# Kernel tuning notes

Hardware: AMD Instinct MI355X
Metric: run time of the kernel (lower is better)

The kernel has to match this reference:

```python
import jax, jax.numpy as jnp
import numpy as np

N = 8192
IN_CH = 256
HID = 256
NEG_INF = -1000000000.0


def setup_inputs() -> dict:
    key = jax.random.key(0)
    ks = jax.random.split(key, 7)
    inlayer = jax.random.normal(ks[0], (N, IN_CH), dtype=jnp.float32)
    adj_mat = jax.random.randint(ks[1], (N, N), 0, 2, dtype=jnp.int32)
    # Xavier-uniform style scales
    s0 = (6.0 / (IN_CH + HID)) ** 0.5
    s1 = (6.0 / (HID + 1)) ** 0.5
    W = jax.random.uniform(ks[2], (HID, IN_CH), jnp.float32, -s0, s0)   # conv1d.weight[:, :, 0]
    w1 = jax.random.uniform(ks[3], (1, HID), jnp.float32, -s1, s1)      # conv1d1.weight[:, :, 0]
    b1 = jax.random.uniform(ks[4], (1,), jnp.float32, -s1, s1)          # conv1d1.bias
    w2 = jax.random.uniform(ks[5], (1, HID), jnp.float32, -s1, s1)      # conv1d2.weight[:, :, 0]
    b2 = jax.random.uniform(ks[6], (1,), jnp.float32, -s1, s1)          # conv1d2.bias
    return {"inlayer": inlayer, "adj_mat": adj_mat, "W": W,
            "w1": w1, "b1": b1, "w2": w2, "b2": b2}


def reference(inlayer, adj_mat, W, w1, b1, w2, b2):
    # 1x1 conv == linear projection: in_fts [HID, N]
    in_fts = W @ inlayer.T
    f1 = (w1 @ in_fts).T + b1          # [N, 1]
    f2 = (w2 @ in_fts).T + b2          # [N, 1]
    logits = f1 + f2.T                 # [N, N] broadcast add
    bias_mat = jnp.where(adj_mat > 0, 0.0, NEG_INF).astype(logits.dtype)
    coefs = jax.nn.softmax(jax.nn.leaky_relu(logits) + bias_mat, axis=-1)
    vals = coefs @ inlayer             # [N, IN_CH]
    return vals
```

## Files before the change

### kernel.cpp

```cpp
#include <hip/hip_runtime.h>
#include <hip/hip_bf16.h>

typedef float f32x4 __attribute__((ext_vector_type(4)));
typedef __bf16 bf16x8 __attribute__((ext_vector_type(8)));

#define N 8192
#define CH 256
#define NJC 4
#define JCW (N / NJC)
#define JT 128
#define NT (JCW / JT)
#define BM 64

static constexpr size_t OFF_P1 = 0;
static constexpr size_t OFF_P2 = 32768;
static constexpr size_t OFF_T1 = 65536;
static constexpr size_t OFF_T2 = 66560;
static constexpr size_t OFF_F1 = 67584;
static constexpr size_t OFF_F2 = OFF_F1 + (size_t)N * 4;
static constexpr size_t OFF_XT = 262144;
static constexpr size_t OFF_SP = OFF_XT + (size_t)CH * N * 2;
static constexpr size_t OFF_PV = OFF_SP + (size_t)NJC * N * 4;

__global__ __launch_bounds__(256) void k1a(
    const float* __restrict__ W, const float* __restrict__ w1,
    const float* __restrict__ w2, float* __restrict__ p1, float* __restrict__ p2)
{
    int b = blockIdx.x, c = threadIdx.x;
    float a1 = 0.f, a2 = 0.f;
#pragma unroll
    for (int hh = 0; hh < 8; ++hh) {
        int h = b * 8 + hh;
        float wv = W[h * CH + c];
        a1 = __builtin_fmaf(w1[h], wv, a1);
        a2 = __builtin_fmaf(w2[h], wv, a2);
    }
    p1[b * CH + c] = a1;
    p2[b * CH + c] = a2;
}

__global__ __launch_bounds__(256) void k1b(
    const float* __restrict__ p1, const float* __restrict__ p2,
    float* __restrict__ t1, float* __restrict__ t2)
{
    int c = threadIdx.x;
    float a1 = 0.f, a2 = 0.f;
#pragma unroll 8
    for (int b = 0; b < 32; ++b) { a1 += p1[b * CH + c]; a2 += p2[b * CH + c]; }
    t1[c] = a1;
    t2[c] = a2;
}

__global__ __launch_bounds__(256) void k2_f(
    const float4* __restrict__ x4, const float* __restrict__ t1,
    const float* __restrict__ t2, const float* __restrict__ b1,
    const float* __restrict__ b2, float* __restrict__ f1, float* __restrict__ f2)
{
    int lane = threadIdx.x & 63, wid = threadIdx.x >> 6;
    int row = blockIdx.x * 4 + wid;
    float4 x = x4[(size_t)row * 64 + lane];
    const float4* t1v = (const float4*)t1;
    const float4* t2v = (const float4*)t2;
    float4 ta = t1v[lane], tb = t2v[lane];
    float d1 = x.x * ta.x + x.y * ta.y + x.z * ta.z + x.w * ta.w;
    float d2 = x.x * tb.x + x.y * tb.y + x.z * tb.z + x.w * tb.w;
#pragma unroll
    for (int off = 32; off; off >>= 1) {
        d1 += __shfl_down(d1, off);
        d2 += __shfl_down(d2, off);
    }
    if (lane == 0) { f1[row] = d1 + b1[0]; f2[row] = d2 + b2[0]; }
}

__global__ __launch_bounds__(256) void kt_pack(
    const float* __restrict__ x, unsigned short* __restrict__ xtp)
{
    __shared__ unsigned short tile[32][264];
    int js32 = blockIdx.x;
    int jb = js32 * 32;
    int t = threadIdx.x;
#pragma unroll
    for (int it = 0; it < 8; ++it) {
        int lin = it * 256 + t;
        int jr = lin >> 6;
        int cq = lin & 63;
        float4 v = *(const float4*)(x + (size_t)(jb + jr) * CH + cq * 4);
        __hip_bfloat16 h0 = __float2bfloat16(v.x);
        __hip_bfloat16 h1 = __float2bfloat16(v.y);
        __hip_bfloat16 h2 = __float2bfloat16(v.z);
        __hip_bfloat16 h3 = __float2bfloat16(v.w);
        tile[jr][cq * 4 + 0] = *(unsigned short*)&h0;
        tile[jr][cq * 4 + 1] = *(unsigned short*)&h1;
        tile[jr][cq * 4 + 2] = *(unsigned short*)&h2;
        tile[jr][cq * 4 + 3] = *(unsigned short*)&h3;
    }
    __syncthreads();
    int lane = t & 63;
    int r = lane & 15, q = lane >> 4;
#pragma unroll
    for (int pass = 0; pass < 4; ++pass) {
        int ct = pass * 4 + (t >> 6);
        unsigned short vs[8];
#pragma unroll
        for (int e = 0; e < 8; ++e) vs[e] = tile[q * 8 + e][ct * 16 + r];
        size_t u = ((size_t)ct * 256 + js32) * 64 + lane;
        *(ulonglong2*)(xtp + u * 8) = *(ulonglong2*)vs;
    }
}

#define BAR() { asm volatile("s_waitcnt lgkmcnt(0)" ::: "memory"); \
                __builtin_amdgcn_s_barrier(); }

__global__ __launch_bounds__(512, 4) void k34_fused(
    const int* __restrict__ adj, const float* __restrict__ f1,
    const float* __restrict__ f2, const unsigned short* __restrict__ xtp,
    float* __restrict__ pv0, float* __restrict__ pvx, float* __restrict__ s_part)
{
    __shared__ __align__(16) unsigned short P[2][BM * JT];
    __shared__ __align__(16) float f2s[JCW];

    const int tid = threadIdx.x;
    const int lane = tid & 63;
    const int w = tid >> 6;
    const int r = lane & 15, q = lane >> 4;
    const int bid = blockIdx.x;
    const int jc = bid & 3;
    const int rb = (bid >> 2) * BM;
    const int jbase = jc * JCW;

    const int prow = tid >> 3;
    const int pjo = (tid & 7) * 16;
    const float f1r = f1[rb + prow];
    const int* aptr = adj + (size_t)(rb + prow) * N + jbase + pjo;
    const int s0i = (tid & 7) * 2;
    const int wu0 = prow * 16 + (s0i ^ (prow & 7));
    const int wu1 = prow * 16 + ((s0i + 1) ^ (prow & 7));

    const unsigned short* xb0 = xtp + (((size_t)(w * 2) * 256 + jc * 64) * 64 + lane) * 8;
    const unsigned short* xb1 = xtp + (((size_t)(w * 2 + 1) * 256 + jc * 64) * 64 + lane) * 8;

    *(float4*)(&f2s[tid * 4]) = *(const float4*)(f2 + jbase + tid * 4);

    f32x4 acc[4][2];
#pragma unroll
    for (int mt = 0; mt < 4; ++mt)
#pragma unroll
        for (int nt = 0; nt < 2; ++nt) acc[mt][nt] = (f32x4){0.f, 0.f, 0.f, 0.f};
    float s_acc = 0.f;

    int4 RA0, RA1, RA2, RA3, RB0, RB1, RB2, RB3;

#define LOAD_A(R0, R1, R2, R3, t)                                   \
    { const int4* p_ = (const int4*)(aptr + (size_t)(t) * JT);      \
      R0 = p_[0]; R1 = p_[1]; R2 = p_[2]; R3 = p_[3]; }
#define EXPW(R0, R1, R2, R3, buf, tt)                               \
    { float4 g0 = *(const float4*)(&f2s[(tt) * JT + pjo]);          \
      float4 g1 = *(const float4*)(&f2s[(tt) * JT + pjo + 4]);      \
      float4 g2 = *(const float4*)(&f2s[(tt) * JT + pjo + 8]);      \
      float4 g3 = *(const float4*)(&f2s[(tt) * JT + pjo + 12]);     \
      int av[16] = {R0.x, R0.y, R0.z, R0.w, R1.x, R1.y, R1.z, R1.w, \
                    R2.x, R2.y, R2.z, R2.w, R3.x, R3.y, R3.z, R3.w};\
      float gv[16] = {g0.x, g0.y, g0.z, g0.w, g1.x, g1.y, g1.z, g1.w,\
                      g2.x, g2.y, g2.z, g2.w, g3.x, g3.y, g3.z, g3.w};\
      bf16x8 pk0, pk1;                                              \
      _Pragma("unroll")                                             \
      for (int e = 0; e < 16; ++e) {                                \
          float t_ = f1r + gv[e];                                   \
          t_ = fmaxf(t_, 0.01f * t_);                               \
          float p_ = (av[e] > 0) ? __expf(t_) : 0.f;                \
          s_acc += p_;                                              \
          if (e < 8) pk0[e] = (__bf16)p_; else pk1[e - 8] = (__bf16)p_; \
      }                                                             \
      *reinterpret_cast<bf16x8*>(&P[buf][(size_t)wu0 * 8]) = pk0;   \
      *reinterpret_cast<bf16x8*>(&P[buf][(size_t)wu1 * 8]) = pk1; }
#define MFMA_TILE(tt, buf)                                          \
    { _Pragma("unroll")                                             \
      for (int kk = 0; kk < 4; ++kk) {                              \
          bf16x8 B0 = *(const bf16x8*)(xb0 + ((size_t)((tt) * 4 + kk) * 64) * 8); \
          bf16x8 B1 = *(const bf16x8*)(xb1 + ((size_t)((tt) * 4 + kk) * 64) * 8); \
          _Pragma("unroll")                                         \
          for (int mt = 0; mt < 4; ++mt) {                          \
              int u_ = (mt * 16 + r) * 16 + ((kk * 4 + q) ^ (r & 7)); \
              bf16x8 A = *(const bf16x8*)(&P[buf][(size_t)u_ * 8]); \
              acc[mt][0] = __builtin_amdgcn_mfma_f32_16x16x32_bf16(A, B0, acc[mt][0], 0, 0, 0); \
              acc[mt][1] = __builtin_amdgcn_mfma_f32_16x16x32_bf16(A, B1, acc[mt][1], 0, 0, 0); \
          }                                                         \
      } }

    LOAD_A(RA0, RA1, RA2, RA3, 0);
    LOAD_A(RB0, RB1, RB2, RB3, 1);
    __syncthreads();
    EXPW(RA0, RA1, RA2, RA3, 0, 0);
    BAR();

    for (int t = 0; t < NT; t += 2) {
        if (t + 2 < NT) LOAD_A(RA0, RA1, RA2, RA3, t + 2);
        MFMA_TILE(t, 0);
        EXPW(RB0, RB1, RB2, RB3, 1, t + 1);
        BAR();
        if (t + 3 < NT) LOAD_A(RB0, RB1, RB2, RB3, t + 3);
        MFMA_TILE(t + 1, 1);
        if (t + 2 < NT) EXPW(RA0, RA1, RA2, RA3, 0, t + 2);
        BAR();
    }

    s_acc += __shfl_xor(s_acc, 1);
    s_acc += __shfl_xor(s_acc, 2);
    s_acc += __shfl_xor(s_acc, 4);
    if ((lane & 7) == 0) s_part[jc * N + rb + prow] = s_acc;

    float* dst = (jc == 0) ? pv0 : (pvx + (size_t)(jc - 1) * N * CH);
#pragma unroll
    for (int mt = 0; mt < 4; ++mt)
#pragma unroll
        for (int nt = 0; nt < 2; ++nt)
#pragma unroll
            for (int reg = 0; reg < 4; ++reg) {
                int row = rb + mt * 16 + q * 4 + reg;
                int col = w * 32 + nt * 16 + r;
                dst[(size_t)row * CH + col] = acc[mt][nt][reg];
            }
#undef LOAD_A
#undef EXPW
#undef MFMA_TILE
}

__global__ __launch_bounds__(256) void k5_reduce(
    const float* __restrict__ pvx, const float* __restrict__ s_part,
    float* __restrict__ out)
{
    int g = blockIdx.x * 256 + threadIdx.x;
    int row = g >> 6;
    float s = s_part[row] + s_part[N + row] + s_part[2 * N + row] + s_part[3 * N + row];
    float inv = (s != 0.f) ? 1.0f / s : 0.f;
    float4* out4 = (float4*)out;
    const float4* p1 = (const float4*)pvx;
    const float4* p2 = p1 + (size_t)N * CH / 4;
    const float4* p3 = p2 + (size_t)N * CH / 4;
    float4 v = out4[g];
    float4 a = p1[g], b = p2[g], c = p3[g];
    v.x = (v.x + a.x + b.x + c.x) * inv;
    v.y = (v.y + a.y + b.y + c.y) * inv;
    v.z = (v.z + a.z + b.z + c.z) * inv;
    v.w = (v.w + a.w + b.w + c.w) * inv;
    out4[g] = v;
}

extern "C" void kernel_launch(void* const* d_in, const int* in_sizes, int n_in,
                              void* d_out, int out_size, void* d_ws, size_t ws_size,
                              hipStream_t stream)
{
    const float* inlayer = (const float*)d_in[0];
    const int*   adj     = (const int*)d_in[1];
    const float* W       = (const float*)d_in[2];
    const float* w1      = (const float*)d_in[3];
    const float* b1      = (const float*)d_in[4];
    const float* w2      = (const float*)d_in[5];
    const float* b2      = (const float*)d_in[6];
    float* out = (float*)d_out;

    char* ws = (char*)d_ws;
    float* p1 = (float*)(ws + OFF_P1);
    float* p2 = (float*)(ws + OFF_P2);
    float* t1 = (float*)(ws + OFF_T1);
    float* t2 = (float*)(ws + OFF_T2);
    float* f1 = (float*)(ws + OFF_F1);
    float* f2 = (float*)(ws + OFF_F2);
    unsigned short* xtp = (unsigned short*)(ws + OFF_XT);
    float* s_part = (float*)(ws + OFF_SP);
    float* pvx = (float*)(ws + OFF_PV);

    k1a<<<dim3(32), dim3(256), 0, stream>>>(W, w1, w2, p1, p2);
    kt_pack<<<dim3(N / 32), dim3(256), 0, stream>>>(inlayer, xtp);
    k1b<<<dim3(1), dim3(256), 0, stream>>>(p1, p2, t1, t2);
    k2_f<<<dim3(N / 4), dim3(256), 0, stream>>>(
        (const float4*)inlayer, t1, t2, b1, b2, f1, f2);
    k34_fused<<<dim3((N / BM) * NJC), dim3(512), 0, stream>>>(
        adj, f1, f2, xtp, out, pvx, s_part);
    k5_reduce<<<dim3(N * CH / 4 / 256), dim3(256), 0, stream>>>(pvx, s_part, out);
}
```

Measured before the change: 110.5 us.

## Fuse f1/f2 projection into transpose-pack kernel and prefetch B tiles in registers

Merges the f1/f2 dot-product kernel into the bf16 transpose-pack kernel, so inlayer is read once and one launch is removed. In the main fused attention kernel, the B operand fragments for the next tile are loaded into registers one stage ahead, overlapping their global-load latency with the current MFMA work. The f2 shared-memory staging is moved after the initial loads. This holds eight more bf16x8 vectors live, raising register pressure, which could hurt occupancy under the 512-thread, 4-block launch bound.

```diff
diff --git a/kernel.cpp b/kernel.cpp
--- a/kernel.cpp
+++ b/kernel.cpp
@@ -51,55 +51,48 @@
     t2[c] = a2;
 }
 
-__global__ __launch_bounds__(256) void k2_f(
-    const float4* __restrict__ x4, const float* __restrict__ t1,
+__global__ __launch_bounds__(256) void ktf(
+    const float* __restrict__ x, const float* __restrict__ t1,
     const float* __restrict__ t2, const float* __restrict__ b1,
-    const float* __restrict__ b2, float* __restrict__ f1, float* __restrict__ f2)
-{
-    int lane = threadIdx.x & 63, wid = threadIdx.x >> 6;
-    int row = blockIdx.x * 4 + wid;
-    float4 x = x4[(size_t)row * 64 + lane];
-    const float4* t1v = (const float4*)t1;
-    const float4* t2v = (const float4*)t2;
-    float4 ta = t1v[lane], tb = t2v[lane];
-    float d1 = x.x * ta.x + x.y * ta.y + x.z * ta.z + x.w * ta.w;
-    float d2 = x.x * tb.x + x.y * tb.y + x.z * tb.z + x.w * tb.w;
-#pragma unroll
-    for (int off = 32; off; off >>= 1) {
-        d1 += __shfl_down(d1, off);
-        d2 += __shfl_down(d2, off);
-    }
-    if (lane == 0) { f1[row] = d1 + b1[0]; f2[row] = d2 + b2[0]; }
-}
-
-__global__ __launch_bounds__(256) void kt_pack(
-    const float* __restrict__ x, unsigned short* __restrict__ xtp)
+    const float* __restrict__ b2, unsigned short* __restrict__ xtp,
+    float* __restrict__ f1, float* __restrict__ f2)
 {
     __shared__ unsigned short tile[32][264];
     int js32 = blockIdx.x;
     int jb = js32 * 32;
     int t = threadIdx.x;
+    int lane = t & 63;
+    int wv = t >> 6;
+    const float4* t1v = (const float4*)t1;
+    const float4* t2v = (const float4*)t2;
+    float4 ta = t1v[lane], tb = t2v[lane];
+    float bb1 = b1[0], bb2 = b2[0];
 #pragma unroll
     for (int it = 0; it < 8; ++it) {
-        int lin = it * 256 + t;
-        int jr = lin >> 6;
-        int cq = lin & 63;
-        float4 v = *(const float4*)(x + (size_t)(jb + jr) * CH + cq * 4);
+        int jr = it * 4 + wv;
+        float4 v = *(const float4*)(x + (size_t)(jb + jr) * CH + lane * 4);
         __hip_bfloat16 h0 = __float2bfloat16(v.x);
         __hip_bfloat16 h1 = __float2bfloat16(v.y);
         __hip_bfloat16 h2 = __float2bfloat16(v.z);
         __hip_bfloat16 h3 = __float2bfloat16(v.w);
-        tile[jr][cq * 4 + 0] = *(unsigned short*)&h0;
-        tile[jr][cq * 4 + 1] = *(unsigned short*)&h1;
-        tile[jr][cq * 4 + 2] = *(unsigned short*)&h2;
-        tile[jr][cq * 4 + 3] = *(unsigned short*)&h3;
+        tile[jr][lane * 4 + 0] = *(unsigned short*)&h0;
+        tile[jr][lane * 4 + 1] = *(unsigned short*)&h1;
+        tile[jr][lane * 4 + 2] = *(unsigned short*)&h2;
+        tile[jr][lane * 4 + 3] = *(unsigned short*)&h3;
+        float d1 = v.x * ta.x + v.y * ta.y + v.z * ta.z + v.w * ta.w;
+        float d2 = v.x * tb.x + v.y * tb.y + v.z * tb.z + v.w * tb.w;
+#pragma unroll
+        for (int off = 32; off; off >>= 1) {
+            d1 += __shfl_down(d1, off);
+            d2 += __shfl_down(d2, off);
+        }
+        if (lane == 0) { f1[jb + jr] = d1 + bb1; f2[jb + jr] = d2 + bb2; }
     }
     __syncthreads();
-    int lane = t & 63;
     int r = lane & 15, q = lane >> 4;
 #pragma unroll
     for (int pass = 0; pass < 4; ++pass) {
-        int ct = pass * 4 + (t >> 6);
+        int ct = pass * 4 + wv;
         unsigned short vs[8];
 #pragma unroll
         for (int e = 0; e < 8; ++e) vs[e] = tile[q * 8 + e][ct * 16 + r];
@@ -139,8 +132,6 @@
     const unsigned short* xb0 = xtp + (((size_t)(w * 2) * 256 + jc * 64) * 64 + lane) * 8;
     const unsigned short* xb1 = xtp + (((size_t)(w * 2 + 1) * 256 + jc * 64) * 64 + lane) * 8;
 
-    *(float4*)(&f2s[tid * 4]) = *(const float4*)(f2 + jbase + tid * 4);
-
     f32x4 acc[4][2];
 #pragma unroll
     for (int mt = 0; mt < 4; ++mt)
@@ -149,10 +140,20 @@
     float s_acc = 0.f;
 
     int4 RA0, RA1, RA2, RA3, RB0, RB1, RB2, RB3;
+    bf16x8 Bv0, Bv1, Bv2, Bv3, Bv4, Bv5, Bv6, Bv7;
 
 #define LOAD_A(R0, R1, R2, R3, t)                                   \
     { const int4* p_ = (const int4*)(aptr + (size_t)(t) * JT);      \
       R0 = p_[0]; R1 = p_[1]; R2 = p_[2]; R3 = p_[3]; }
+#define LOAD_B(tt)                                                  \
+    { Bv0 = *(const bf16x8*)(xb0 + ((size_t)((tt) * 4 + 0) * 64) * 8); \
+      Bv1 = *(const bf16x8*)(xb0 + ((size_t)((tt) * 4 + 1) * 64) * 8); \
+      Bv2 = *(const bf16x8*)(xb0 + ((size_t)((tt) * 4 + 2) * 64) * 8); \
+      Bv3 = *(const bf16x8*)(xb0 + ((size_t)((tt) * 4 + 3) * 64) * 8); \
+      Bv4 = *(const bf16x8*)(xb1 + ((size_t)((tt) * 4 + 0) * 64) * 8); \
+      Bv5 = *(const bf16x8*)(xb1 + ((size_t)((tt) * 4 + 1) * 64) * 8); \
+      Bv6 = *(const bf16x8*)(xb1 + ((size_t)((tt) * 4 + 2) * 64) * 8); \
+      Bv7 = *(const bf16x8*)(xb1 + ((size_t)((tt) * 4 + 3) * 64) * 8); }
 #define EXPW(R0, R1, R2, R3, buf, tt)                               \
     { float4 g0 = *(const float4*)(&f2s[(tt) * JT + pjo]);          \
       float4 g1 = *(const float4*)(&f2s[(tt) * JT + pjo + 4]);      \
@@ -173,11 +174,11 @@
       }                                                             \
       *reinterpret_cast<bf16x8*>(&P[buf][(size_t)wu0 * 8]) = pk0;   \
       *reinterpret_cast<bf16x8*>(&P[buf][(size_t)wu1 * 8]) = pk1; }
-#define MFMA_TILE(tt, buf)                                          \
+#define MFMA_TILE(buf)                                              \
     { _Pragma("unroll")                                             \
       for (int kk = 0; kk < 4; ++kk) {                              \
-          bf16x8 B0 = *(const bf16x8*)(xb0 + ((size_t)((tt) * 4 + kk) * 64) * 8); \
-          bf16x8 B1 = *(const bf16x8*)(xb1 + ((size_t)((tt) * 4 + kk) * 64) * 8); \
+          bf16x8 B0 = (kk == 0) ? Bv0 : (kk == 1) ? Bv1 : (kk == 2) ? Bv2 : Bv3; \
+          bf16x8 B1 = (kk == 0) ? Bv4 : (kk == 1) ? Bv5 : (kk == 2) ? Bv6 : Bv7; \
           _Pragma("unroll")                                         \
           for (int mt = 0; mt < 4; ++mt) {                          \
               int u_ = (mt * 16 + r) * 16 + ((kk * 4 + q) ^ (r & 7)); \
@@ -189,17 +190,21 @@
 
     LOAD_A(RA0, RA1, RA2, RA3, 0);
     LOAD_A(RB0, RB1, RB2, RB3, 1);
+    LOAD_B(0);
+    *(float4*)(&f2s[tid * 4]) = *(const float4*)(f2 + jbase + tid * 4);
     __syncthreads();
     EXPW(RA0, RA1, RA2, RA3, 0, 0);
     BAR();
 
     for (int t = 0; t < NT; t += 2) {
+        MFMA_TILE(0);
+        LOAD_B(t + 1);
         if (t + 2 < NT) LOAD_A(RA0, RA1, RA2, RA3, t + 2);
-        MFMA_TILE(t, 0);
         EXPW(RB0, RB1, RB2, RB3, 1, t + 1);
         BAR();
+        MFMA_TILE(1);
+        if (t + 2 < NT) LOAD_B(t + 2);
         if (t + 3 < NT) LOAD_A(RB0, RB1, RB2, RB3, t + 3);
-        MFMA_TILE(t + 1, 1);
         if (t + 2 < NT) EXPW(RA0, RA1, RA2, RA3, 0, t + 2);
         BAR();
     }
@@ -221,6 +226,7 @@
                 dst[(size_t)row * CH + col] = acc[mt][nt][reg];
             }
 #undef LOAD_A
+#undef LOAD_B
 #undef EXPW
 #undef MFMA_TILE
 }
@@ -271,10 +277,9 @@
     float* pvx = (float*)(ws + OFF_PV);
 
     k1a<<<dim3(32), dim3(256), 0, stream>>>(W, w1, w2, p1, p2);
-    kt_pack<<<dim3(N / 32), dim3(256), 0, stream>>>(inlayer, xtp);
     k1b<<<dim3(1), dim3(256), 0, stream>>>(p1, p2, t1, t2);
-    k2_f<<<dim3(N / 4), dim3(256), 0, stream>>>(
-        (const float4*)inlayer, t1, t2, b1, b2, f1, f2);
+    ktf<<<dim3(N / 32), dim3(256), 0, stream>>>(
+        inlayer, t1, t2, b1, b2, xtp, f1, f2);
     k34_fused<<<dim3((N / BM) * NJC), dim3(512), 0, stream>>>(
         adj, f1, f2, xtp, out, pvx, s_part);
     k5_reduce<<<dim3(N * CH / 4 / 256), dim3(256), 0, stream>>>(pvx, s_part, out);
```

Result: slower. 154.3 us (+39.6%).
